# Kernel tuning notes

Measured on AMD Instinct MI355X. Metric: run time of the kernel, lower is better.

The kernel has to match this reference:

```python
import jax, jax.numpy as jnp
import numpy as np

N = 100000   # total nodes across all graphs
E = 1600000  # edges (avg degree 16)
D = 128      # input feature dim
H = 64       # hidden dim
B = 8        # number of graphs
EPS = 1e-5   # BatchNorm eps


def setup_inputs() -> dict:
    key = jax.random.key(0)
    ks = jax.random.split(key, 12)
    x = jax.random.normal(ks[0], (N, D), dtype=jnp.float32)
    edge_index = jax.random.randint(ks[1], (2, E), 0, N, dtype=jnp.int64)
    batch = jnp.sort(jax.random.randint(ks[2], (N,), 0, B, dtype=jnp.int64))
    s1 = 1.0 / np.sqrt(D)
    s2 = 1.0 / np.sqrt(H)
    W1l = jax.random.uniform(ks[3], (D, H), minval=-s1, maxval=s1, dtype=jnp.float32)
    W1r = jax.random.uniform(ks[4], (D, H), minval=-s1, maxval=s1, dtype=jnp.float32)
    b1 = jnp.zeros((H,), jnp.float32)
    gamma1 = jnp.ones((H,), jnp.float32)
    beta1 = jnp.zeros((H,), jnp.float32)
    W2l = jax.random.uniform(ks[5], (H, H), minval=-s2, maxval=s2, dtype=jnp.float32)
    W2r = jax.random.uniform(ks[6], (H, H), minval=-s2, maxval=s2, dtype=jnp.float32)
    b2 = jnp.zeros((H,), jnp.float32)
    return {"x": x, "edge_index": edge_index, "batch": batch,
            "W1l": W1l, "b1": b1, "W1r": W1r, "gamma1": gamma1, "beta1": beta1,
            "W2l": W2l, "b2": b2, "W2r": W2r}


def _seg_mean(vals, idx, num):
    # scatter-mean: sum per segment / count, zero-degree segments give 0 (count clamped)
    s = jax.ops.segment_sum(vals, idx, num_segments=num)
    cnt = jax.ops.segment_sum(jnp.ones((idx.shape[0], 1), vals.dtype), idx, num_segments=num)
    return s / jnp.maximum(cnt, 1.0)


def reference(x, edge_index, batch, W1l, b1, W1r, gamma1, beta1, W2l, b2, W2r):
    src, dst = edge_index[0], edge_index[1]
    # SAGEConv layer 1: mean-aggregate neighbors, lin_l(agg) + lin_r(x)
    agg1 = _seg_mean(x[src], dst, N)            # [N, D]
    h = agg1 @ W1l + b1 + x @ W1r               # [N, H]
    # BatchNorm1d (training-mode batch stats, biased var) then ReLU
    mu = jnp.mean(h, axis=0)
    var = jnp.var(h, axis=0)
    h = (h - mu) * jax.lax.rsqrt(var + EPS) * gamma1 + beta1
    h = jax.nn.relu(h)
    # SAGEConv layer 2 (no norm/act after last layer)
    agg2 = _seg_mean(h[src], dst, N)            # [N, H]
    h2 = agg2 @ W2l + b2 + h @ W2r              # [N, H]
    # per-graph global mean pool -> [B, H]
    return _seg_mean(h2, batch, B)
```

## Files before the change

kernel.cpp:

```cpp
#include <hip/hip_runtime.h>

#define N_NODES 100000
#define E_EDGES 1600000
#define DIM 128
#define HID 64
#define NGRAPH 8
#define EPSBN 1e-5f

#define GSHIFT 9
#define GNODES (1 << GSHIFT)
#define NGROUP ((N_NODES + GNODES - 1) >> GSHIFT)
#define GCAP 10240
#define CHUNK 2048
#define PBLK 256
#define EPT (CHUNK / PBLK)
#define NCHUNK ((E_EDGES + CHUNK - 1) / CHUNK)
#define MM1B ((N_NODES + 63) / 64)
#define GATB 2048

#if __has_builtin(__builtin_amdgcn_cvt_pk_fp8_f32) && \
    __has_builtin(__builtin_amdgcn_cvt_pk_f32_fp8)
#define HW_FP8 1
#else
#define HW_FP8 0
#endif

typedef float floatx2 __attribute__((ext_vector_type(2)));
typedef short bf16x8 __attribute__((ext_vector_type(8)));
typedef float f32x4 __attribute__((ext_vector_type(4)));

__device__ __forceinline__ unsigned f2bf_pack(float lo, float hi) {
  unsigned ul = __float_as_uint(lo);
  unsigned uh = __float_as_uint(hi);
  ul = (ul + 0x7fffu + ((ul >> 16) & 1u)) >> 16;
  uh = (uh + 0x7fffu + ((uh >> 16) & 1u)) >> 16;
  return (uh << 16) | ul;
}
__device__ __forceinline__ float bflo(unsigned u) {
  return __uint_as_float(u << 16);
}
__device__ __forceinline__ float bfhi(unsigned u) {
  return __uint_as_float(u & 0xffff0000u);
}

#if !HW_FP8
__device__ __forceinline__ unsigned char f32_to_e4m3(float f) {
  unsigned u = __float_as_uint(f);
  unsigned s = (u >> 24) & 0x80u;
  float a = fabsf(f);
  if (a >= 464.f) return (unsigned char)(s | 0x7E);
  if (a < 0.015625f) {
    int m = (int)rintf(a * 512.f);
    if (m >= 8) return (unsigned char)(s | 0x08);
    return (unsigned char)(s | (unsigned)m);
  }
  int e = (int)((u >> 23) & 0xFF) - 127;
  float q = ldexpf(a, -e) * 8.f;
  int m = (int)rintf(q);
  if (m == 16) { m = 8; ++e; }
  if (e > 8) return (unsigned char)(s | 0x7E);
  return (unsigned char)(s | (unsigned)(((e + 7) << 3) | (m - 8)));
}
#endif

__device__ __forceinline__ unsigned pack4_e4m3(float a, float b, float c,
                                               float d) {
#if HW_FP8
  int w = __builtin_amdgcn_cvt_pk_fp8_f32(a, b, 0, false);
  w = __builtin_amdgcn_cvt_pk_fp8_f32(c, d, w, true);
  return (unsigned)w;
#else
  return (unsigned)f32_to_e4m3(a) | ((unsigned)f32_to_e4m3(b) << 8) |
         ((unsigned)f32_to_e4m3(c) << 16) | ((unsigned)f32_to_e4m3(d) << 24);
#endif
}

__global__ __launch_bounds__(64) void wprep_kernel(
    const float* __restrict__ W1l, const float* __restrict__ W1r,
    unsigned* __restrict__ wTbf) {
  int n = blockIdx.x;
  int kp = threadIdx.x;
  const float* Wc = (n < 64) ? (W1l + n) : (W1r + (n - 64));
  float w0 = Wc[(size_t)(2 * kp) * HID];
  float w1 = Wc[(size_t)(2 * kp + 1) * HID];
  wTbf[n * 64 + kp] = f2bf_pack(w0, w1);
}

__global__ __launch_bounds__(PBLK) void part_mm1_kernel(
    const int* __restrict__ src, const int* __restrict__ dst,
    int* __restrict__ gcnt, unsigned* __restrict__ part,
    const float* __restrict__ x, const unsigned* __restrict__ wTbf,
    unsigned char* __restrict__ y1f8, unsigned* __restrict__ y2bf) {
  __shared__ __align__(16) unsigned char smraw[52224];

  if (blockIdx.x < NCHUNK) {
    int* hist = (int*)(smraw);
    int* sc = (int*)(smraw + 1024);
    int* scanoff = (int*)(smraw + 2048);
    int* gbase = (int*)(smraw + 3072);
    unsigned* buf = (unsigned*)(smraw + 4096);
    unsigned char* gid = smraw + 12288;

    int c = blockIdx.x;
    int e0 = c * CHUNK;
    int m = E_EDGES - e0;
    m = m < CHUNK ? m : CHUNK;
    int t = threadIdx.x;

    hist[t] = 0;
    __syncthreads();

    int myg[EPT];
    unsigned mytok[EPT];
    int myrank[EPT];
    #pragma unroll
    for (int q = 0; q < EPT; ++q) {
      int i = t + q * PBLK;
      if (i < m) {
        int d = dst[e0 + i];
        int s = src[e0 + i];
        int g = d >> GSHIFT;
        myg[q] = g;
        mytok[q] = ((unsigned)(d & (GNODES - 1)) << 17) | (unsigned)s;
        myrank[q] = atomicAdd(&hist[g], 1);
      } else {
        myg[q] = -1;
      }
    }
    __syncthreads();

    sc[t] = hist[t];
    if (t < NGROUP && hist[t] > 0) gbase[t] = atomicAdd(&gcnt[t], hist[t]);
    __syncthreads();
    for (int off = 1; off < 256; off <<= 1) {
      int add = (t >= off) ? sc[t - off] : 0;
      __syncthreads();
      sc[t] += add;
      __syncthreads();
    }
    scanoff[t] = sc[t] - hist[t];
    __syncthreads();

    #pragma unroll
    for (int q = 0; q < EPT; ++q) {
      if (myg[q] >= 0) {
        int pos = scanoff[myg[q]] + myrank[q];
        buf[pos] = mytok[q];
        gid[pos] = (unsigned char)myg[q];
      }
    }
    __syncthreads();

    for (int i = t; i < m; i += PBLK) {
      int g = gid[i];
      int addr = gbase[g] + (i - scanoff[g]);
      if (addr < GCAP) part[(size_t)g * GCAP + addr] = buf[i];
    }
  } else {
    short* xs = (short*)smraw;
    short* wts = (short*)(smraw + 17408);
    int t = threadIdx.x;
    int brow = (blockIdx.x - NCHUNK) * 64;

    for (int i = t; i < 64 * 32; i += PBLK) {
      int r = i >> 5;
      int c4 = (i & 31) << 2;
      int n = brow + r;
      unsigned lo = 0u, hi = 0u;
      if (n < N_NODES) {
        float4 v = *reinterpret_cast<const float4*>(x + (size_t)n * DIM + c4);
        lo = f2bf_pack(v.x, v.y);
        hi = f2bf_pack(v.z, v.w);
      }
      unsigned* dp = (unsigned*)(xs + r * 136 + c4);
      dp[0] = lo;
      dp[1] = hi;
    }
    for (int i = t; i < 128 * 64; i += PBLK) {
      int nn = i >> 6;
      int kp = i & 63;
      *(unsigned*)(wts + nn * 136 + kp * 2) = wTbf[i];
    }
    __syncthreads();

    int lane = t & 63;
    int w = t >> 6;
    int l15 = lane & 15;
    int lg = lane >> 4;

    f32x4 acc[8];
    #pragma unroll
    for (int j = 0; j < 8; ++j) acc[j] = (f32x4){0.f, 0.f, 0.f, 0.f};

    #pragma unroll
    for (int ks = 0; ks < 4; ++ks) {
      int k0 = ks * 32 + lg * 8;
      bf16x8 a = *(const bf16x8*)(xs + (w * 16 + l15) * 136 + k0);
      #pragma unroll
      for (int nf = 0; nf < 8; ++nf) {
        bf16x8 b = *(const bf16x8*)(wts + (nf * 16 + l15) * 136 + k0);
        acc[nf] =
            __builtin_amdgcn_mfma_f32_16x16x32_bf16(a, b, acc[nf], 0, 0, 0);
      }
    }
    __syncthreads();

    float* osm = (float*)smraw;
    #pragma unroll
    for (int nf = 0; nf < 8; ++nf) {
      int col = nf * 16 + l15;
      int r0 = w * 16 + lg * 4;
      #pragma unroll
      for (int rg = 0; rg < 4; ++rg)
        osm[(r0 + rg) * 132 + col] = acc[nf][rg];
    }
    __syncthreads();

    int r = t & 63;
    int cq = (t >> 6) << 4;
    int n = brow + r;
    if (n < N_NODES) {
      const float* a1 = osm + r * 132 + cq;
      const float* a2 = osm + r * 132 + 64 + cq;
      uint4 pk;
      pk.x = pack4_e4m3(a1[0], a1[1], a1[2], a1[3]);
      pk.y = pack4_e4m3(a1[4], a1[5], a1[6], a1[7]);
      pk.z = pack4_e4m3(a1[8], a1[9], a1[10], a1[11]);
      pk.w = pack4_e4m3(a1[12], a1[13], a1[14], a1[15]);
      *reinterpret_cast<uint4*>(y1f8 + (size_t)n * HID + cq) = pk;

      uint4 q0, q1;
      q0.x = f2bf_pack(a2[0], a2[1]);
      q0.y = f2bf_pack(a2[2], a2[3]);
      q0.z = f2bf_pack(a2[4], a2[5]);
      q0.w = f2bf_pack(a2[6], a2[7]);
      q1.x = f2bf_pack(a2[8], a2[9]);
      q1.y = f2bf_pack(a2[10], a2[11]);
      q1.z = f2bf_pack(a2[12], a2[13]);
      q1.w = f2bf_pack(a2[14], a2[15]);
      unsigned* ob = y2bf + (size_t)n * (HID / 2) + (cq >> 1);
      reinterpret_cast<uint4*>(ob)[0] = q0;
      reinterpret_cast<uint4*>(ob)[1] = q1;
    }
  }
}

__global__ __launch_bounds__(512) void groupcsr_kernel(
    const int* __restrict__ gcnt, const unsigned* __restrict__ part,
    const int* __restrict__ batch, int* __restrict__ rowptr,
    int* __restrict__ csr, unsigned* __restrict__ tok2) {
  __shared__ int hist[GNODES];
  __shared__ int excl[GNODES];
  __shared__ int degl[GNODES];
  __shared__ int batl[GNODES];
  __shared__ int sc2[256];
  int g = blockIdx.x;
  int t = threadIdx.x;

  if (t < 256) sc2[t] = (t < NGROUP) ? min(gcnt[t], GCAP) : 0;
  __syncthreads();
  for (int off = 1; off < 256; off <<= 1) {
    int add = (t < 256 && t >= off) ? sc2[t - off] : 0;
    __syncthreads();
    if (t < 256) sc2[t] += add;
    __syncthreads();
  }
  int gbase = (g > 0) ? sc2[g - 1] : 0;

  hist[t] = 0;
  {
    int n = (g << GSHIFT) + t;
    batl[t] = (n < N_NODES) ? batch[n] : 0;
  }
  __syncthreads();

  int cnt = min(gcnt[g], GCAP);
  const unsigned* ga = part + (size_t)g * GCAP;
  for (int i = t; i < cnt; i += 512) atomicAdd(&hist[ga[i] >> 17], 1);
  __syncthreads();

  int orig = hist[t];
  degl[t] = orig;
  for (int off = 1; off < GNODES; off <<= 1) {
    int add = (t >= off) ? hist[t - off] : 0;
    __syncthreads();
    hist[t] += add;
    __syncthreads();
  }
  excl[t] = hist[t] - orig;
  __syncthreads();

  int n = (g << GSHIFT) + t;
  if (n <= N_NODES) rowptr[n] = gbase + excl[t];
  if (g == 0 && t == 0) rowptr[0] = 0;
  __syncthreads();

  for (int i = t; i < cnt; i += 512) {
    unsigned p = ga[i];
    int dloc = (int)(p >> 17);
    int pos = gbase + atomicAdd(&excl[dloc], 1);
    unsigned s = p & 0x1FFFFu;
    csr[pos] = (int)s;
    unsigned dg = (unsigned)degl[dloc];
    if (dg > 1023u) dg = 1023u;
    tok2[pos] = (dg << 20) | ((unsigned)batl[dloc] << 17) | s;
  }
}

__global__ __launch_bounds__(PBLK) void part2_gather_kernel(
    const unsigned* __restrict__ tok2, int* __restrict__ gcnt2,
    unsigned* __restrict__ part2, const uint2* __restrict__ yf8,
    const int* __restrict__ csr, const int* __restrict__ rowptr,
    const unsigned* __restrict__ otherbf, const float* __restrict__ bias,
    unsigned* __restrict__ outCbf, float* __restrict__ stats) {
  __shared__ int hist[256];
  __shared__ int sc[256];
  __shared__ int scanoff[256];
  __shared__ int gbase[256];
  __shared__ unsigned buf[CHUNK];
  __shared__ unsigned char gid[CHUNK];
  __shared__ float ss[HID];
  __shared__ float sq[HID];

  if (blockIdx.x < NCHUNK) {
    int c = blockIdx.x;
    int e0 = c * CHUNK;
    int m = E_EDGES - e0;
    m = m < CHUNK ? m : CHUNK;
    int t = threadIdx.x;

    hist[t] = 0;
    __syncthreads();

    int myg[EPT];
    unsigned mytok[EPT];
    int myrank[EPT];
    #pragma unroll
    for (int q = 0; q < EPT; ++q) {
      int i = t + q * PBLK;
      if (i < m) {
        unsigned p = tok2[e0 + i];
        int g = (int)((p & 0x1FFFFu) >> GSHIFT);
        myg[q] = g;
        mytok[q] = p;
        myrank[q] = atomicAdd(&hist[g], 1);
      } else {
        myg[q] = -1;
      }
    }
    __syncthreads();

    sc[t] = hist[t];
    if (t < NGROUP && hist[t] > 0) gbase[t] = atomicAdd(&gcnt2[t], hist[t]);
    __syncthreads();
    for (int off = 1; off < 256; off <<= 1) {
      int add = (t >= off) ? sc[t - off] : 0;
      __syncthreads();
      sc[t] += add;
      __syncthreads();
    }
    scanoff[t] = sc[t] - hist[t];
    __syncthreads();

    #pragma unroll
    for (int q = 0; q < EPT; ++q) {
      if (myg[q] >= 0) {
        int pos = scanoff[myg[q]] + myrank[q];
        buf[pos] = mytok[q];
        gid[pos] = (unsigned char)myg[q];
      }
    }
    __syncthreads();

    for (int i = t; i < m; i += PBLK) {
      int g = gid[i];
      int addr = gbase[g] + (i - scanoff[g]);
      if (addr < GCAP) part2[(size_t)g * GCAP + addr] = buf[i];
    }
  } else {
#if !HW_FP8
    __shared__ float tbl[256];
    {
      int t = threadIdx.x;
      if (t < 256) {
        int e = (t >> 3) & 15;
        int m = t & 7;
        float v = e ? ldexpf((float)(8 + m), e - 10) : ldexpf((float)m, -9);
        tbl[t] = (t & 0x80) ? -v : v;
      }
    }
    __syncthreads();
#endif
    int lane = threadIdx.x & 63;
    int oct = lane >> 3;
    int lo = lane & 7;
    int gbid = blockIdx.x - NCHUNK;
    int wid = (gbid * PBLK + (int)threadIdx.x) >> 6;
    const int nw = (GATB * PBLK) >> 6;

    float bj[8];
    #pragma unroll
    for (int k = 0; k < 8; ++k) bj[k] = bias[lo * 8 + k];

    float ls[8], lq[8];
    #pragma unroll
    for (int k = 0; k < 8; ++k) { ls[k] = 0.f; lq[k] = 0.f; }

    for (int nb = wid * 8; nb < N_NODES; nb += nw * 8) {
      int n = nb + oct;
      bool valid = n < N_NODES;
      int start = valid ? rowptr[n] : 0;
      int end = valid ? rowptr[n + 1] : 0;

      float acc[8];
      #pragma unroll
      for (int k = 0; k < 8; ++k) acc[k] = 0.f;

      for (int bse = start; bse < end; bse += 8) {
        int m = end - bse;
        m = m < 8 ? m : 8;
        int e = bse + lo;
        int s = (e < end) ? csr[e] : 0;
        uint2 vv[8];
        #pragma unroll
        for (int i = 0; i < 8; ++i) {
          int si = __shfl(s, i, 8);
          vv[i] = yf8[(size_t)si * 8 + lo];
        }
        #pragma unroll
        for (int i = 0; i < 8; ++i) {
          if (i < m) {
#if HW_FP8
            floatx2 p0 = __builtin_amdgcn_cvt_pk_f32_fp8((int)vv[i].x, false);
            floatx2 p1 = __builtin_amdgcn_cvt_pk_f32_fp8((int)vv[i].x, true);
            floatx2 p2 = __builtin_amdgcn_cvt_pk_f32_fp8((int)vv[i].y, false);
            floatx2 p3 = __builtin_amdgcn_cvt_pk_f32_fp8((int)vv[i].y, true);
            acc[0] += p0[0];
            acc[1] += p0[1];
            acc[2] += p1[0];
            acc[3] += p1[1];
            acc[4] += p2[0];
            acc[5] += p2[1];
            acc[6] += p3[0];
            acc[7] += p3[1];
#else
            acc[0] += tbl[vv[i].x & 255u];
            acc[1] += tbl[(vv[i].x >> 8) & 255u];
            acc[2] += tbl[(vv[i].x >> 16) & 255u];
            acc[3] += tbl[vv[i].x >> 24];
            acc[4] += tbl[vv[i].y & 255u];
            acc[5] += tbl[(vv[i].y >> 8) & 255u];
            acc[6] += tbl[(vv[i].y >> 16) & 255u];
            acc[7] += tbl[vv[i].y >> 24];
#endif
          }
        }
      }

      if (valid) {
        int deg = end - start;
        float inv = 1.f / (float)(deg > 1 ? deg : 1);
        uint4 ov = *reinterpret_cast<const uint4*>(otherbf +
                                                   (size_t)n * (HID / 2) +
                                                   lo * 4);
        float v[8];
        v[0] = fmaf(acc[0], inv, bj[0]) + bflo(ov.x);
        v[1] = fmaf(acc[1], inv, bj[1]) + bfhi(ov.x);
        v[2] = fmaf(acc[2], inv, bj[2]) + bflo(ov.y);
        v[3] = fmaf(acc[3], inv, bj[3]) + bfhi(ov.y);
        v[4] = fmaf(acc[4], inv, bj[4]) + bflo(ov.z);
        v[5] = fmaf(acc[5], inv, bj[5]) + bfhi(ov.z);
        v[6] = fmaf(acc[6], inv, bj[6]) + bflo(ov.w);
        v[7] = fmaf(acc[7], inv, bj[7]) + bfhi(ov.w);
        uint4 cw4;
        cw4.x = f2bf_pack(v[0], v[1]);
        cw4.y = f2bf_pack(v[2], v[3]);
        cw4.z = f2bf_pack(v[4], v[5]);
        cw4.w = f2bf_pack(v[6], v[7]);
        *reinterpret_cast<uint4*>(outCbf + (size_t)n * (HID / 2) + lo * 4) =
            cw4;
        #pragma unroll
        for (int k = 0; k < 8; ++k) {
          ls[k] += v[k];
          lq[k] = fmaf(v[k], v[k], lq[k]);
        }
      }
    }

    int t = threadIdx.x;
    if (t < HID) { ss[t] = 0.f; sq[t] = 0.f; }
    __syncthreads();
    #pragma unroll
    for (int k = 0; k < 8; ++k) {
      atomicAdd(&ss[lo * 8 + k], ls[k]);
      atomicAdd(&sq[lo * 8 + k], lq[k]);
    }
    __syncthreads();
    if (t < HID) {
      unsafeAtomicAdd(&stats[t], ss[t]);
      unsafeAtomicAdd(&stats[HID + t], sq[t]);
    }
  }
}

__global__ __launch_bounds__(256) void chsum_kernel(
    const int* __restrict__ gcnt2, const unsigned* __restrict__ part2,
    const unsigned* __restrict__ Cbf, const float* __restrict__ stats,
    const float* __restrict__ gamma, const float* __restrict__ beta,
    const int* __restrict__ batch, float* __restrict__ S1g,
    float* __restrict__ S2g) {
  __shared__ float c[GNODES * NGRAPH];
  __shared__ float r1[HID * NGRAPH];
  __shared__ float r2[HID * NGRAPH];
  int g = blockIdx.x;
  int t = threadIdx.x;

  for (int i = t; i < GNODES * NGRAPH; i += 256) c[i] = 0.f;
  for (int i = t; i < HID * NGRAPH; i += 256) { r1[i] = 0.f; r2[i] = 0.f; }
  __syncthreads();

  int cnt = min(gcnt2[g], GCAP);
  const unsigned* ga = part2 + (size_t)g * GCAP;
  for (int i = t; i < cnt; i += 256) {
    unsigned p = ga[i];
    int sl = (int)(p & (GNODES - 1));
    int b = (int)((p >> 17) & 7u);
    int deg = (int)((p >> 20) & 0x3FFu);
    float w = 1.f / (float)(deg > 1 ? deg : 1);
    atomicAdd(&c[sl * NGRAPH + b], w);
  }
  __syncthreads();

  int lane = t & 63;
  int wv = t >> 6;

  float inv_n = 1.0f / (float)N_NODES;
  float mu = stats[lane] * inv_n;
  float var = stats[HID + lane] * inv_n - mu * mu;
  float scl = gamma[lane] * rsqrtf(var + EPSBN);
  float shf = beta[lane] - mu * scl;

  float s1[NGRAPH], s2[NGRAPH];
  #pragma unroll
  for (int b = 0; b < NGRAPH; ++b) { s1[b] = 0.f; s2[b] = 0.f; }

  int nend = N_NODES - (g << GSHIFT);
  nend = nend < GNODES ? nend : GNODES;
  for (int nl = wv; nl < nend; nl += 4) {
    int n = (g << GSHIFT) + nl;
    unsigned u = Cbf[(size_t)n * (HID / 2) + (lane >> 1)];
    float hr = (lane & 1) ? bfhi(u) : bflo(u);
    float h = fmaf(hr, scl, shf);
    h = h > 0.f ? h : 0.f;
    int bn = batch[n];
    #pragma unroll
    for (int b = 0; b < NGRAPH; ++b) {
      float cb = c[nl * NGRAPH + b];
      s1[b] = fmaf(cb, h, s1[b]);
      s2[b] += (b == bn) ? h : 0.f;
    }
  }

  #pragma unroll
  for (int b = 0; b < NGRAPH; ++b) {
    atomicAdd(&r1[b * HID + lane], s1[b]);
    atomicAdd(&r2[b * HID + lane], s2[b]);
  }
  __syncthreads();
  for (int i = t; i < HID * NGRAPH; i += 256) {
    unsafeAtomicAdd(&S1g[i], r1[i]);
    unsafeAtomicAdd(&S2g[i], r2[i]);
  }
}

__device__ __forceinline__ int lbound(const int* __restrict__ a, int key) {
  int lo = 0, hi = N_NODES;
  while (lo < hi) {
    int mid = (lo + hi) >> 1;
    if (a[mid] < key) lo = mid + 1; else hi = mid;
  }
  return lo;
}

__global__ __launch_bounds__(512) void finale_kernel(
    const float* __restrict__ S1g, const float* __restrict__ S2g,
    const int* __restrict__ batch, const float* __restrict__ W2l,
    const float* __restrict__ W2r, const float* __restrict__ b2,
    float* __restrict__ out) {
  int t = threadIdx.x;
  int b = t >> 6;
  int oc = t & 63;
  int V = lbound(batch, b + 1) - lbound(batch, b);
  float acc = 0.f;
  for (int k = 0; k < HID; ++k) {
    acc = fmaf(S1g[b * HID + k], W2l[k * HID + oc], acc);
    acc = fmaf(S2g[b * HID + k], W2r[k * HID + oc], acc);
  }
  out[t] = (V > 0) ? (acc / (float)V + b2[oc]) : 0.f;
}

extern "C" void kernel_launch(void* const* d_in, const int* in_sizes, int n_in,
                              void* d_out, int out_size, void* d_ws,
                              size_t ws_size, hipStream_t stream) {
  const float* x      = (const float*)d_in[0];
  const int*   ei     = (const int*)d_in[1];
  const int*   batch  = (const int*)d_in[2];
  const float* W1l    = (const float*)d_in[3];
  const float* b1     = (const float*)d_in[4];
  const float* W1r    = (const float*)d_in[5];
  const float* gamma1 = (const float*)d_in[6];
  const float* beta1  = (const float*)d_in[7];
  const float* W2l    = (const float*)d_in[8];
  const float* b2     = (const float*)d_in[9];
  const float* W2r    = (const float*)d_in[10];

  const int* src = ei;
  const int* dst = ei + E_EDGES;

  float* ws = (float*)d_ws;
  size_t off = 0;
  unsigned char* Af8 = (unsigned char*)(ws + off);
  off += (size_t)N_NODES * HID / 4;
  unsigned* Bbf = (unsigned*)(ws + off);
  off += (size_t)N_NODES * (HID / 2);
  unsigned* Cbf = (unsigned*)(ws + off);
  off += (size_t)N_NODES * (HID / 2);
  int* gcnt     = (int*)(ws + off); off += 256;
  int* gcnt2    = (int*)(ws + off); off += 256;
  float* stats  = ws + off; off += 2 * HID;
  float* S1g    = ws + off; off += NGRAPH * HID;
  float* S2g    = ws + off; off += NGRAPH * HID;
  size_t zero_elems = 256 + 256 + 2 * HID + 2 * NGRAPH * HID;
  unsigned* wTbf = (unsigned*)(ws + off); off += 128 * 64;
  int* rowptr   = (int*)(ws + off); off += N_NODES + 1;
  int* csr      = (int*)(ws + off); off += E_EDGES;
  unsigned* tok2 = (unsigned*)(ws + off); off += E_EDGES;
  unsigned* part = (unsigned*)(ws + off); off += (size_t)NGROUP * GCAP;

  hipMemsetAsync(gcnt, 0, zero_elems * sizeof(float), stream);

  wprep_kernel<<<128, 64, 0, stream>>>(W1l, W1r, wTbf);

  part_mm1_kernel<<<NCHUNK + MM1B, PBLK, 0, stream>>>(
      src, dst, gcnt, part, x, wTbf, Af8, Bbf);

  groupcsr_kernel<<<NGROUP, 512, 0, stream>>>(gcnt, part, batch, rowptr, csr,
                                              tok2);

  part2_gather_kernel<<<NCHUNK + GATB, PBLK, 0, stream>>>(
      tok2, gcnt2, part, (const uint2*)Af8, csr, rowptr, Bbf, b1, Cbf, stats);

  chsum_kernel<<<NGROUP, 256, 0, stream>>>(gcnt2, part, Cbf, stats, gamma1,
                                           beta1, batch, S1g, S2g);

  finale_kernel<<<1, 512, 0, stream>>>(S1g, S2g, batch, W2l, W2r, b2,
                                       (float*)d_out);
}
```

Baseline: 242.4 us.

## Write MFMA accumulators directly in permuted column layout and read weights from global

The node-transform GEMM no longer stages weights in shared memory or round-trips accumulators through an LDS output tile. Each lane writes its accumulator values straight to the fp8 and bf16 intermediate buffers in a permuted column order, and downstream kernels (gather bias, BN/pool, finale) remap channels through colOfPos to match. This cuts LDS footprint (raising occupancy of the fused partition/GEMM kernel) and removes two barriers, at the cost of narrower global stores and per-lane weight loads from global/L2.

```diff
diff --git a/kernel.cpp b/kernel.cpp
--- a/kernel.cpp
+++ b/kernel.cpp
@@ -29,6 +29,10 @@
 typedef short bf16x8 __attribute__((ext_vector_type(8)));
 typedef float f32x4 __attribute__((ext_vector_type(4)));
 
+__device__ __forceinline__ int colOfPos(int p) {
+  return 16 * (p & 3) + (p >> 2);
+}
+
 __device__ __forceinline__ unsigned f2bf_pack(float lo, float hi) {
   unsigned ul = __float_as_uint(lo);
   unsigned uh = __float_as_uint(hi);
@@ -91,7 +95,7 @@
     int* __restrict__ gcnt, unsigned* __restrict__ part,
     const float* __restrict__ x, const unsigned* __restrict__ wTbf,
     unsigned char* __restrict__ y1f8, unsigned* __restrict__ y2bf) {
-  __shared__ __align__(16) unsigned char smraw[52224];
+  __shared__ __align__(16) unsigned char smraw[17536];
 
   if (blockIdx.x < NCHUNK) {
     int* hist = (int*)(smraw);
@@ -158,7 +162,6 @@
     }
   } else {
     short* xs = (short*)smraw;
-    short* wts = (short*)(smraw + 17408);
     int t = threadIdx.x;
     int brow = (blockIdx.x - NCHUNK) * 64;
 
@@ -176,11 +179,6 @@
       dp[0] = lo;
       dp[1] = hi;
     }
-    for (int i = t; i < 128 * 64; i += PBLK) {
-      int nn = i >> 6;
-      int kp = i & 63;
-      *(unsigned*)(wts + nn * 136 + kp * 2) = wTbf[i];
-    }
     __syncthreads();
 
     int lane = t & 63;
@@ -196,51 +194,35 @@
     for (int ks = 0; ks < 4; ++ks) {
       int k0 = ks * 32 + lg * 8;
       bf16x8 a = *(const bf16x8*)(xs + (w * 16 + l15) * 136 + k0);
+      bf16x8 bfr[8];
       #pragma unroll
       for (int nf = 0; nf < 8; ++nf) {
-        bf16x8 b = *(const bf16x8*)(wts + (nf * 16 + l15) * 136 + k0);
+        const uint4* bp = reinterpret_cast<const uint4*>(
+            wTbf + (nf * 16 + l15) * 64 + ks * 16 + lg * 4);
+        uint4 bv = *bp;
+        bfr[nf] = *(const bf16x8*)&bv;
+      }
+      #pragma unroll
+      for (int nf = 0; nf < 8; ++nf)
         acc[nf] =
-            __builtin_amdgcn_mfma_f32_16x16x32_bf16(a, b, acc[nf], 0, 0, 0);
-      }
-    }
-    __syncthreads();
-
-    float* osm = (float*)smraw;
-    #pragma unroll
-    for (int nf = 0; nf < 8; ++nf) {
-      int col = nf * 16 + l15;
-      int r0 = w * 16 + lg * 4;
-      #pragma unroll
-      for (int rg = 0; rg < 4; ++rg)
-        osm[(r0 + rg) * 132 + col] = acc[nf][rg];
-    }
-    __syncthreads();
-
-    int r = t & 63;
-    int cq = (t >> 6) << 4;
-    int n = brow + r;
-    if (n < N_NODES) {
-      const float* a1 = osm + r * 132 + cq;
-      const float* a2 = osm + r * 132 + 64 + cq;
-      uint4 pk;
-      pk.x = pack4_e4m3(a1[0], a1[1], a1[2], a1[3]);
-      pk.y = pack4_e4m3(a1[4], a1[5], a1[6], a1[7]);
-      pk.z = pack4_e4m3(a1[8], a1[9], a1[10], a1[11]);
-      pk.w = pack4_e4m3(a1[12], a1[13], a1[14], a1[15]);
-      *reinterpret_cast<uint4*>(y1f8 + (size_t)n * HID + cq) = pk;
-
-      uint4 q0, q1;
-      q0.x = f2bf_pack(a2[0], a2[1]);
-      q0.y = f2bf_pack(a2[2], a2[3]);
-      q0.z = f2bf_pack(a2[4], a2[5]);
-      q0.w = f2bf_pack(a2[6], a2[7]);
-      q1.x = f2bf_pack(a2[8], a2[9]);
-      q1.y = f2bf_pack(a2[10], a2[11]);
-      q1.z = f2bf_pack(a2[12], a2[13]);
-      q1.w = f2bf_pack(a2[14], a2[15]);
-      unsigned* ob = y2bf + (size_t)n * (HID / 2) + (cq >> 1);
-      reinterpret_cast<uint4*>(ob)[0] = q0;
-      reinterpret_cast<uint4*>(ob)[1] = q1;
+            __builtin_amdgcn_mfma_f32_16x16x32_bf16(a, bfr[nf], acc[nf], 0,
+                                                    0, 0);
+    }
+
+    #pragma unroll
+    for (int rg = 0; rg < 4; ++rg) {
+      int r = w * 16 + lg * 4 + rg;
+      int n = brow + r;
+      if (n < N_NODES) {
+        unsigned p1 = pack4_e4m3(acc[0][rg], acc[1][rg], acc[2][rg],
+                                 acc[3][rg]);
+        *reinterpret_cast<unsigned*>(y1f8 + (size_t)n * HID + l15 * 4) = p1;
+        uint2 p2;
+        p2.x = f2bf_pack(acc[4][rg], acc[5][rg]);
+        p2.y = f2bf_pack(acc[6][rg], acc[7][rg]);
+        *reinterpret_cast<uint2*>(y2bf + (size_t)n * (HID / 2) + l15 * 2) =
+            p2;
+      }
     }
   }
 }
@@ -400,7 +382,7 @@
 
     float bj[8];
     #pragma unroll
-    for (int k = 0; k < 8; ++k) bj[k] = bias[lo * 8 + k];
+    for (int k = 0; k < 8; ++k) bj[k] = bias[colOfPos(lo * 8 + k)];
 
     float ls[8], lq[8];
     #pragma unroll
@@ -533,12 +515,13 @@
 
   int lane = t & 63;
   int wv = t >> 6;
+  int cl = colOfPos(lane);
 
   float inv_n = 1.0f / (float)N_NODES;
   float mu = stats[lane] * inv_n;
   float var = stats[HID + lane] * inv_n - mu * mu;
-  float scl = gamma[lane] * rsqrtf(var + EPSBN);
-  float shf = beta[lane] - mu * scl;
+  float scl = gamma[cl] * rsqrtf(var + EPSBN);
+  float shf = beta[cl] - mu * scl;
 
   float s1[NGRAPH], s2[NGRAPH];
   #pragma unroll
@@ -592,9 +575,10 @@
   int oc = t & 63;
   int V = lbound(batch, b + 1) - lbound(batch, b);
   float acc = 0.f;
-  for (int k = 0; k < HID; ++k) {
-    acc = fmaf(S1g[b * HID + k], W2l[k * HID + oc], acc);
-    acc = fmaf(S2g[b * HID + k], W2r[k * HID + oc], acc);
+  for (int l = 0; l < HID; ++l) {
+    int k = colOfPos(l);
+    acc = fmaf(S1g[b * HID + l], W2l[k * HID + oc], acc);
+    acc = fmaf(S2g[b * HID + l], W2r[k * HID + oc], acc);
   }
   out[t] = (V > 0) ? (acc / (float)V + b2[oc]) : 0.f;
 }
```

Measured after the change: 254.9 us. 5.2% more time.
